# Kernel tuning notes

Measured on AMD Instinct MI355X. Metric: run time of the kernel, lower is better.

Reference implementation:

```python
import jax, jax.numpy as jnp
import numpy as np

CUTOFF = 2.0
LOG2 = float(np.log(2.0))

def ssp(x):
    # shifted softplus: softplus(x) - log(2)
    return jax.nn.softplus(x) - LOG2

def setup_inputs() -> dict:
    key = jax.random.key(0)
    ks = jax.random.split(key, 12)
    N, E, H, F, G = 10000, 320000, 256, 256, 50
    x = jax.random.normal(ks[0], (N, H), dtype=jnp.float32)
    edge_index = jax.random.randint(ks[1], (2, E), 0, N, dtype=jnp.int64)
    edge_weight = jax.random.normal(ks[2], (E, 3), dtype=jnp.float32)
    edge_attr = jax.random.normal(ks[3], (E, G), dtype=jnp.float32)
    s = lambda fan_in: 1.0 / np.sqrt(fan_in)
    mlp_w1 = jax.random.uniform(ks[4], (G, F), jnp.float32, -s(G), s(G))
    mlp_b1 = jax.random.uniform(ks[5], (F,), jnp.float32, -s(G), s(G))
    mlp_w2 = jax.random.uniform(ks[6], (F, F), jnp.float32, -s(F), s(F))
    mlp_b2 = jax.random.uniform(ks[7], (F,), jnp.float32, -s(F), s(F))
    lin1_w = jax.random.uniform(ks[8], (H, F), jnp.float32, -s(H), s(H))
    lin2_w = jax.random.uniform(ks[9], (F, H), jnp.float32, -s(F), s(F))
    lin2_b = jax.random.uniform(ks[10], (H,), jnp.float32, -s(F), s(F))
    return {"x": x, "edge_index": edge_index, "edge_weight": edge_weight,
            "edge_attr": edge_attr, "mlp_w1": mlp_w1, "mlp_b1": mlp_b1,
            "mlp_w2": mlp_w2, "mlp_b2": mlp_b2, "lin1_w": lin1_w,
            "lin2_w": lin2_w, "lin2_b": lin2_b}

def reference(x, edge_index, edge_weight, edge_attr,
              mlp_w1, mlp_b1, mlp_w2, mlp_b2, lin1_w, lin2_w, lin2_b):
    N = x.shape[0]
    # cutoff envelope on edge distances
    distances = jnp.linalg.norm(edge_weight, axis=1)                 # [E]
    C = 0.5 * (jnp.cos(distances * jnp.pi / CUTOFF) + 1.0)
    C = C * (distances <= CUTOFF)                                    # [E]
    # edge filter MLP
    W = ssp(edge_attr @ mlp_w1 + mlp_b1) @ mlp_w2 + mlp_b2           # [E, F]
    W = W * C[:, None]
    i, j = edge_index[0], edge_index[1]
    messages = W * (x[j] @ lin1_w)                                   # [E, F]
    agg = jax.ops.segment_sum(messages, i, num_segments=N)           # [N, F]
    h = ssp(agg @ lin2_w + lin2_b)                                   # [N, H]
    return x + h
```

## Files before the change

kernel.cpp:

```cpp
#include <hip/hip_runtime.h>
#include <hip/hip_bf16.h>
#include <stdint.h>

#define HF 256
#define GG 50

typedef __attribute__((ext_vector_type(8))) short bf16x8;
typedef __attribute__((ext_vector_type(4))) short bf16x4;
typedef __attribute__((ext_vector_type(4))) float f32x4;

__device__ __forceinline__ uint32_t f2bf2u(float a, float b){
    __hip_bfloat162 h = __float22bfloat162_rn(make_float2(a, b));
    union { __hip_bfloat162 h; uint32_t u; } v; v.h = h; return v.u;
}
__device__ __forceinline__ short f2bf(float x){
    union { float f; uint32_t u; } v; v.f = x;
    uint32_t r = (v.u + 0x7FFFu + ((v.u >> 16) & 1u)) >> 16;
    return (short)(uint16_t)r;
}
__device__ __forceinline__ float bf2f(short s){
    union { uint32_t u; float f; } v; v.u = ((uint32_t)(uint16_t)s) << 16;
    return v.f;
}
__device__ __forceinline__ float ssp_f(float x){
    return fmaxf(x, 0.f) + __logf(1.f + __expf(-fabsf(x))) - 0.69314718055994531f;
}

__device__ __forceinline__ void pack_natural(const float* __restrict__ B,
                                             short* __restrict__ Bp,
                                             int idx, int KT, int kmax)
{
    int lane = idx & 63;
    int kt   = (idx >> 6) & (KT - 1);
    int ntg  = idx >> (6 + (KT == 2 ? 1 : 3));
    int col  = ntg * 16 + (lane & 15);
    int k0   = kt * 32 + (lane >> 4) * 8;
    uint32_t u[4];
#pragma unroll
    for (int jj = 0; jj < 4; ++jj) {
        int ka = k0 + 2*jj, kb = k0 + 2*jj + 1;
        float a = (ka < kmax) ? B[(size_t)ka * HF + col] : 0.f;
        float b = (kb < kmax) ? B[(size_t)kb * HF + col] : 0.f;
        u[jj] = f2bf2u(a, b);
    }
    *(uint4*)&Bp[(size_t)idx * 8] = *(uint4*)u;
}

__global__ __launch_bounds__(256)
void prep_kernel(const float* __restrict__ w1, const float* __restrict__ w2,
                 const float* __restrict__ lin1, const float* __restrict__ lin2,
                 short* __restrict__ w1p, short* __restrict__ w2p,
                 short* __restrict__ lin1p, short* __restrict__ lin2p,
                 const float* __restrict__ x, short* __restrict__ x_bf, int nx8,
                 const int* __restrict__ eidx, int* __restrict__ cnt, int E, int gConv)
{
    int b = blockIdx.x, tid = threadIdx.x;
    if (b < 8) {
        pack_natural(w1, w1p, b * 256 + tid, 2, GG);
    } else if (b < 40) {
        int idx = (b - 8) * 256 + tid;
        int lane = idx & 63;
        int kt   = (idx >> 6) & 7;
        int ntg  = idx >> 9;
        int col  = ntg * 16 + (lane & 15);
        int s0   = kt * 32 + (lane >> 4) * 8;
        uint32_t u[4];
#pragma unroll
        for (int jj = 0; jj < 4; ++jj) {
            int sa = s0 + 2*jj, sb = sa + 1;
            int fa = (sa >> 6) * 64 + (sa & 3) * 16 + ((sa & 63) >> 2);
            int fb = (sb >> 6) * 64 + (sb & 3) * 16 + ((sb & 63) >> 2);
            u[jj] = f2bf2u(w2[(size_t)fa * HF + col], w2[(size_t)fb * HF + col]);
        }
        *(uint4*)&w2p[(size_t)idx * 8] = *(uint4*)u;
    } else if (b < 72) {
        pack_natural(lin1, lin1p, (b - 40) * 256 + tid, 8, HF);
    } else if (b < 104) {
        pack_natural(lin2, lin2p, (b - 72) * 256 + tid, 8, HF);
    } else if (b < 104 + gConv) {
        int idx = (b - 104) * 256 + tid;
        if (idx < nx8) {
            const float* xp = x + (size_t)idx * 8;
            float4 p0 = *(const float4*)(xp);
            float4 p1 = *(const float4*)(xp + 4);
            uint32_t u[4] = { f2bf2u(p0.x, p0.y), f2bf2u(p0.z, p0.w),
                              f2bf2u(p1.x, p1.y), f2bf2u(p1.z, p1.w) };
            *(uint4*)&x_bf[(size_t)idx * 8] = *(uint4*)u;
        }
    } else {
        int e = (b - 104 - gConv) * 256 + tid;
        if (e < E) atomicAdd(&cnt[eidx[e]], 1);
    }
}

__global__ __launch_bounds__(256)
void scan_kernel(const int* __restrict__ cnt, int* __restrict__ row,
                 int* __restrict__ cursor, int N, int E)
{
    __shared__ int part[256];
    const int t = threadIdx.x;
    const int CH = (N + 255) / 256;
    int lo = t * CH;
    int hi = min(lo + CH, N);
    int s = 0;
    for (int n = lo; n < hi; ++n) s += cnt[n];
    part[t] = s;
    __syncthreads();
    for (int off = 1; off < 256; off <<= 1) {
        int v = (t >= off) ? part[t - off] : 0;
        __syncthreads();
        part[t] += v;
        __syncthreads();
    }
    int acc = part[t] - s;
    for (int n = lo; n < hi; ++n) {
        row[n] = acc; cursor[n] = acc;
        acc += cnt[n];
    }
    if (t == 255) row[N] = E;
}

__global__ __launch_bounds__(256)
void mid_kernel(const int* __restrict__ eidx, int* __restrict__ cursor,
                int* __restrict__ perm, int E, int gScatter,
                const short* __restrict__ x_bf, const short* __restrict__ lin1p,
                short* __restrict__ y_p, int N)
{
    const int tid = threadIdx.x;
    if ((int)blockIdx.x < gScatter) {
        int e = blockIdx.x * 256 + tid;
        if (e < E) {
            int pos = atomicAdd(&cursor[eidx[e]], 1);
            perm[pos] = e;
        }
        return;
    }
    const int blk  = blockIdx.x - gScatter;
    const int lane = tid & 63;
    const int w    = tid >> 6;
    const int l15  = lane & 15;
    const int quad = lane >> 4;
    const int row0 = blk * 64;

    f32x4 acc[4][4];
#pragma unroll
    for (int mt = 0; mt < 4; ++mt)
#pragma unroll
        for (int nt = 0; nt < 4; ++nt)
            acc[mt][nt] = (f32x4){0.f, 0.f, 0.f, 0.f};

#pragma unroll 2
    for (int kt = 0; kt < 8; ++kt) {
        bf16x8 af[4];
#pragma unroll
        for (int mt = 0; mt < 4; ++mt) {
            int r = row0 + mt * 16 + l15;
            int rl = (r < N) ? r : 0;
            af[mt] = *(const bf16x8*)&x_bf[(size_t)rl * HF + kt * 32 + quad * 8];
        }
#pragma unroll
        for (int nt = 0; nt < 4; ++nt) {
            bf16x8 bfr = *(const bf16x8*)&lin1p[(size_t)(((w * 4 + nt) * 8 + kt) * 64 + lane) * 8];
#pragma unroll
            for (int mt = 0; mt < 4; ++mt)
                acc[mt][nt] = __builtin_amdgcn_mfma_f32_16x16x32_bf16(af[mt], bfr, acc[mt][nt], 0, 0, 0);
        }
    }
#pragma unroll
    for (int mt = 0; mt < 4; ++mt) {
#pragma unroll
        for (int r = 0; r < 4; ++r) {
            int row = row0 + mt * 16 + quad * 4 + r;
            if (row < N) {
                uint2 u = make_uint2(f2bf2u(acc[mt][0][r], acc[mt][1][r]),
                                     f2bf2u(acc[mt][2][r], acc[mt][3][r]));
                *(uint2*)&y_p[(size_t)row * HF + w * 64 + l15 * 4] = u;
            }
        }
    }
}

__global__ __launch_bounds__(256)
void node2_kernel(const float* __restrict__ agg, const short* __restrict__ lin2p,
                  const float* __restrict__ bias, const float* __restrict__ x,
                  float* __restrict__ out, int N)
{
    const int tid  = threadIdx.x;
    const int lane = tid & 63;
    const int w    = tid >> 6;
    const int l15  = lane & 15;
    const int quad = lane >> 4;
    const int row0 = blockIdx.x * 64;

    f32x4 acc[4][4];
#pragma unroll
    for (int mt = 0; mt < 4; ++mt)
#pragma unroll
        for (int nt = 0; nt < 4; ++nt)
            acc[mt][nt] = (f32x4){0.f, 0.f, 0.f, 0.f};

#pragma unroll 2
    for (int kt = 0; kt < 8; ++kt) {
        bf16x8 af[4];
#pragma unroll
        for (int mt = 0; mt < 4; ++mt) {
            int r = row0 + mt * 16 + l15;
            int rl = (r < N) ? r : 0;
            const float* ap = agg + (size_t)rl * HF + kt * 32 + quad * 8;
            float4 p0 = *(const float4*)(ap);
            float4 p1 = *(const float4*)(ap + 4);
            union { uint32_t u[4]; bf16x8 v; } c;
            c.u[0] = f2bf2u(p0.x, p0.y); c.u[1] = f2bf2u(p0.z, p0.w);
            c.u[2] = f2bf2u(p1.x, p1.y); c.u[3] = f2bf2u(p1.z, p1.w);
            af[mt] = c.v;
        }
#pragma unroll
        for (int nt = 0; nt < 4; ++nt) {
            bf16x8 bfr = *(const bf16x8*)&lin2p[(size_t)(((w * 4 + nt) * 8 + kt) * 64 + lane) * 8];
#pragma unroll
            for (int mt = 0; mt < 4; ++mt)
                acc[mt][nt] = __builtin_amdgcn_mfma_f32_16x16x32_bf16(af[mt], bfr, acc[mt][nt], 0, 0, 0);
        }
    }
    float bs[4];
#pragma unroll
    for (int nt = 0; nt < 4; ++nt) bs[nt] = bias[w * 64 + nt * 16 + l15];
#pragma unroll
    for (int mt = 0; mt < 4; ++mt) {
#pragma unroll
        for (int r = 0; r < 4; ++r) {
            int row = row0 + mt * 16 + quad * 4 + r;
            if (row < N) {
#pragma unroll
                for (int nt = 0; nt < 4; ++nt) {
                    int f = w * 64 + nt * 16 + l15;
                    float v = ssp_f(acc[mt][nt][r] + bs[nt]) + x[(size_t)row * HF + f];
                    out[(size_t)row * HF + f] = v;
                }
            }
        }
    }
}

__global__ __launch_bounds__(256, 3)
void edge_mfma(const float* __restrict__ ea, const int* __restrict__ eidx,
               const float* __restrict__ ew,
               const short* __restrict__ w1p, const float* __restrict__ b1,
               const short* __restrict__ w2p, const float* __restrict__ b2,
               const short* __restrict__ y_p, const int* __restrict__ perm,
               const int* __restrict__ rowp,
               float* __restrict__ agg, int E)
{
    __shared__ short smem[21504];
    short* ea_b = smem;
    short* hid  = smem + 4608;
    short* msgT = smem;
    __shared__ int s_e[64], s_i[64], s_j[64];
    __shared__ float s_c[64];
    __shared__ unsigned long long s_bmask;

    const int tid  = threadIdx.x;
    const int lane = tid & 63;
    const int w    = tid >> 6;
    const int l15  = lane & 15;
    const int quad = lane >> 4;
    const int e0   = blockIdx.x * 64;

    if (tid < 64) {
        int p = e0 + tid;
        int e = 0, iv = -1, jv = 0;
        float c = 0.f;
        if (p < E) {
            e  = perm[p];
            iv = eidx[e];
            jv = eidx[E + e];
            float d0 = ew[e*3+0], d1 = ew[e*3+1], d2 = ew[e*3+2];
            float d = sqrtf(d0*d0 + d1*d1 + d2*d2);
            c = (d <= 2.0f) ? 0.5f * (__cosf(d * 1.57079632679489662f) + 1.0f) : 0.f;
        }
        s_e[tid] = e; s_i[tid] = iv; s_j[tid] = jv; s_c[tid] = c;
        int ivn = __shfl_down(iv, 1);
        bool flag = (tid == 63) || (iv != ivn);
        unsigned long long m = __ballot(flag);
        if (tid == 0) s_bmask = m;
    }
    __syncthreads();

    for (int idx = tid; idx < 64 * 25; idx += 256) {
        int e = idx / 25, p = idx - e * 25;
        const float* sp = ea + (size_t)s_e[e] * GG + p * 2;
        float2 v = *(const float2*)sp;
        *(uint32_t*)&ea_b[e * 72 + p * 2] = f2bf2u(v.x, v.y);
    }
    for (int idx = tid; idx < 64 * 7; idx += 256) {
        int e = idx / 7, q = idx - e * 7;
        *(uint32_t*)&ea_b[e * 72 + 50 + q * 2] = 0u;
    }
    __syncthreads();

    f32x4 acc1[4][4];
#pragma unroll
    for (int mt = 0; mt < 4; ++mt)
#pragma unroll
        for (int nt = 0; nt < 4; ++nt)
            acc1[mt][nt] = (f32x4){0.f, 0.f, 0.f, 0.f};

#pragma unroll
    for (int kt = 0; kt < 2; ++kt) {
        bf16x8 af[4];
#pragma unroll
        for (int mt = 0; mt < 4; ++mt)
            af[mt] = *(bf16x8*)&ea_b[(mt * 16 + l15) * 72 + kt * 32 + quad * 8];
#pragma unroll
        for (int nt = 0; nt < 4; ++nt) {
            bf16x8 bfr = *(const bf16x8*)&w1p[(size_t)(((w * 4 + nt) * 2 + kt) * 64 + lane) * 8];
#pragma unroll
            for (int mt = 0; mt < 4; ++mt)
                acc1[mt][nt] = __builtin_amdgcn_mfma_f32_16x16x32_bf16(af[mt], bfr, acc1[mt][nt], 0, 0, 0);
        }
    }

    float bias1[4];
#pragma unroll
    for (int nt = 0; nt < 4; ++nt) bias1[nt] = b1[w * 64 + nt * 16 + l15];
#pragma unroll
    for (int mt = 0; mt < 4; ++mt) {
#pragma unroll
        for (int r = 0; r < 4; ++r) {
            int e = mt * 16 + quad * 4 + r;
            float v0 = ssp_f(acc1[mt][0][r] + bias1[0]);
            float v1 = ssp_f(acc1[mt][1][r] + bias1[1]);
            float v2 = ssp_f(acc1[mt][2][r] + bias1[2]);
            float v3 = ssp_f(acc1[mt][3][r] + bias1[3]);
            uint2 u = make_uint2(f2bf2u(v0, v1), f2bf2u(v2, v3));
            *(uint2*)&hid[e * 264 + w * 64 + l15 * 4] = u;
        }
    }
    __syncthreads();

    bf16x4 yv[4][4];
#pragma unroll
    for (int mt = 0; mt < 4; ++mt)
#pragma unroll
        for (int r = 0; r < 4; ++r) {
            int e = mt * 16 + quad * 4 + r;
            yv[mt][r] = *(const bf16x4*)&y_p[(size_t)s_j[e] * HF + w * 64 + l15 * 4];
        }

    f32x4 acc2[4][4];
#pragma unroll
    for (int mt = 0; mt < 4; ++mt)
#pragma unroll
        for (int nt = 0; nt < 4; ++nt)
            acc2[mt][nt] = (f32x4){0.f, 0.f, 0.f, 0.f};

#pragma unroll 2
    for (int kt = 0; kt < 8; ++kt) {
        bf16x8 af[4];
#pragma unroll
        for (int mt = 0; mt < 4; ++mt)
            af[mt] = *(bf16x8*)&hid[(mt * 16 + l15) * 264 + kt * 32 + quad * 8];
#pragma unroll
        for (int nt = 0; nt < 4; ++nt) {
            bf16x8 bfr = *(const bf16x8*)&w2p[(size_t)(((w * 4 + nt) * 8 + kt) * 64 + lane) * 8];
#pragma unroll
            for (int mt = 0; mt < 4; ++mt)
                acc2[mt][nt] = __builtin_amdgcn_mfma_f32_16x16x32_bf16(af[mt], bfr, acc2[mt][nt], 0, 0, 0);
        }
    }
    __syncthreads();

    float bias2[4];
#pragma unroll
    for (int nt = 0; nt < 4; ++nt) bias2[nt] = b2[w * 64 + nt * 16 + l15];
    float cs[4][4];
#pragma unroll
    for (int mt = 0; mt < 4; ++mt)
#pragma unroll
        for (int r = 0; r < 4; ++r)
            cs[mt][r] = s_c[mt * 16 + quad * 4 + r];
#pragma unroll
    for (int mt = 0; mt < 4; ++mt) {
#pragma unroll
        for (int nt = 0; nt < 4; ++nt) {
            int col = w * 64 + nt * 16 + l15;
            float v0 = (acc2[mt][nt][0] + bias2[nt]) * cs[mt][0] * bf2f(yv[mt][0][nt]);
            float v1 = (acc2[mt][nt][1] + bias2[nt]) * cs[mt][1] * bf2f(yv[mt][1][nt]);
            float v2 = (acc2[mt][nt][2] + bias2[nt]) * cs[mt][2] * bf2f(yv[mt][2][nt]);
            float v3 = (acc2[mt][nt][3] + bias2[nt]) * cs[mt][3] * bf2f(yv[mt][3][nt]);
            uint2 u = make_uint2(f2bf2u(v0, v1), f2bf2u(v2, v3));
            *(uint2*)&msgT[col * 68 + mt * 16 + quad * 4] = u;
        }
    }
    __syncthreads();

    {
        unsigned long long bm = s_bmask;
        unsigned mlo = __builtin_amdgcn_readfirstlane((unsigned)bm);
        unsigned mhi = __builtin_amdgcn_readfirstlane((unsigned)(bm >> 32));
        const int col = tid;
        float sum = 0.f;
#pragma unroll
        for (int ch = 0; ch < 8; ++ch) {
            bf16x8 v = *(bf16x8*)&msgT[col * 68 + ch * 8];
#pragma unroll
            for (int j = 0; j < 8; ++j) {
                int e = ch * 8 + j;
                sum += bf2f(v[j]);
                unsigned bit = (e < 32) ? ((mlo >> e) & 1u) : ((mhi >> (e - 32)) & 1u);
                if (bit) {
                    int node = __builtin_amdgcn_readfirstlane(s_i[e]);
                    if (node >= 0) {
                        int lo = rowp[node], hi = rowp[node + 1];
                        float* ap = agg + (size_t)node * HF + col;
                        if (lo >= e0 && hi <= e0 + 64) *ap = sum;
                        else atomicAdd(ap, sum);
                    }
                    sum = 0.f;
                }
            }
        }
    }
}

extern "C" void kernel_launch(void* const* d_in, const int* in_sizes, int n_in,
                              void* d_out, int out_size, void* d_ws, size_t ws_size,
                              hipStream_t stream)
{
    const float* x     = (const float*)d_in[0];
    const int*   eidx  = (const int*)  d_in[1];
    const float* ew    = (const float*)d_in[2];
    const float* ea    = (const float*)d_in[3];
    const float* w1    = (const float*)d_in[4];
    const float* b1    = (const float*)d_in[5];
    const float* w2    = (const float*)d_in[6];
    const float* b2    = (const float*)d_in[7];
    const float* lin1  = (const float*)d_in[8];
    const float* lin2  = (const float*)d_in[9];
    const float* lin2b = (const float*)d_in[10];
    float* out = (float*)d_out;

    const int N = in_sizes[0] / HF;
    const int E = in_sizes[2] / 3;

    const size_t fN = (size_t)N * HF;
    float* agg    = (float*)d_ws;
    short* y_p    = (short*)(agg + fN);
    short* x_bf   = y_p + fN;
    int*   cnt    = (int*)(x_bf + fN);
    int*   row    = cnt + N;
    int*   cursor = row + (N + 8);
    int*   perm   = cursor + N;
    short* w1p    = (short*)(((uintptr_t)(perm + E) + 255) & ~(uintptr_t)255);
    short* w2p    = w1p + 16384;
    short* lin1p  = w2p + 65536;
    short* lin2p  = lin1p + 65536;

    hipMemsetAsync(cnt, 0, (size_t)N * sizeof(int), stream);
    hipMemsetAsync(agg, 0, fN * sizeof(float), stream);

    const int nx8   = (int)(fN / 8);
    const int gConv = (nx8 + 255) / 256;
    const int gHist = (E + 255) / 256;
    prep_kernel<<<dim3(104 + gConv + gHist), dim3(256), 0, stream>>>(
        w1, w2, lin1, lin2, w1p, w2p, lin1p, lin2p, x, x_bf, nx8, eidx, cnt, E, gConv);

    scan_kernel<<<dim3(1), dim3(256), 0, stream>>>(cnt, row, cursor, N, E);

    const int gScatter = (E + 255) / 256;
    const int gNode    = (N + 63) / 64;
    mid_kernel<<<dim3(gScatter + gNode), dim3(256), 0, stream>>>(
        eidx, cursor, perm, E, gScatter, x_bf, lin1p, y_p, N);

    edge_mfma<<<dim3((E + 63) / 64), dim3(256), 0, stream>>>(
        ea, eidx, ew, w1p, b1, w2p, b2, y_p, perm, row, agg, E);

    node2_kernel<<<dim3(gNode), dim3(256), 0, stream>>>(
        agg, lin2p, lin2b, x, out, N);
}
```

Measured before the change: 346.6 us.

## Do segment reduction with MFMA selection matrix and fold agg zeroing into prep

Replaces the per-column serial scan over 64 edges, which did scalar atomics or stores at each run boundary, with an MFMA product of the transposed message tile and a 0/1 run-selection matrix built in shared memory. Each run's sum then comes out of the matrix unit and is written as float4 stores, or atomics when the run crosses the block. Run node ids and a completeness flag are precomputed per block. The separate memset of agg is folded into the prep kernel as extra zeroing blocks, removing one launch. This adds an extra loop iteration with barriers whenever a block holds more than 16 runs, and random node ids likely give many runs per 64 edges, so the new path may do more work than the old scan.

```diff
diff --git a/kernel.cpp b/kernel.cpp
--- a/kernel.cpp
+++ b/kernel.cpp
@@ -12,11 +12,6 @@
 __device__ __forceinline__ uint32_t f2bf2u(float a, float b){
     __hip_bfloat162 h = __float22bfloat162_rn(make_float2(a, b));
     union { __hip_bfloat162 h; uint32_t u; } v; v.h = h; return v.u;
-}
-__device__ __forceinline__ short f2bf(float x){
-    union { float f; uint32_t u; } v; v.f = x;
-    uint32_t r = (v.u + 0x7FFFu + ((v.u >> 16) & 1u)) >> 16;
-    return (short)(uint16_t)r;
 }
 __device__ __forceinline__ float bf2f(short s){
     union { uint32_t u; float f; } v; v.u = ((uint32_t)(uint16_t)s) << 16;
@@ -38,7 +33,7 @@
     uint32_t u[4];
 #pragma unroll
     for (int jj = 0; jj < 4; ++jj) {
-        int ka = k0 + 2*jj, kb = k0 + 2*jj + 1;
+        int ka = k0 + 2*jj, kb = ka + 1;
         float a = (ka < kmax) ? B[(size_t)ka * HF + col] : 0.f;
         float b = (kb < kmax) ? B[(size_t)kb * HF + col] : 0.f;
         u[jj] = f2bf2u(a, b);
@@ -52,7 +47,8 @@
                  short* __restrict__ w1p, short* __restrict__ w2p,
                  short* __restrict__ lin1p, short* __restrict__ lin2p,
                  const float* __restrict__ x, short* __restrict__ x_bf, int nx8,
-                 const int* __restrict__ eidx, int* __restrict__ cnt, int E, int gConv)
+                 const int* __restrict__ eidx, int* __restrict__ cnt, int E,
+                 float* __restrict__ agg, int nAgg4, int gConv, int gHist)
 {
     int b = blockIdx.x, tid = threadIdx.x;
     if (b < 8) {
@@ -87,9 +83,12 @@
                               f2bf2u(p1.x, p1.y), f2bf2u(p1.z, p1.w) };
             *(uint4*)&x_bf[(size_t)idx * 8] = *(uint4*)u;
         }
-    } else {
+    } else if (b < 104 + gConv + gHist) {
         int e = (b - 104 - gConv) * 256 + tid;
         if (e < E) atomicAdd(&cnt[eidx[e]], 1);
+    } else {
+        int idx = (b - 104 - gConv - gHist) * 256 + tid;
+        if (idx < nAgg4) ((float4*)agg)[idx] = make_float4(0.f, 0.f, 0.f, 0.f);
     }
 }
 
@@ -146,8 +145,7 @@
 #pragma unroll
     for (int mt = 0; mt < 4; ++mt)
 #pragma unroll
-        for (int nt = 0; nt < 4; ++nt)
-            acc[mt][nt] = (f32x4){0.f, 0.f, 0.f, 0.f};
+        for (int nt = 0; nt < 4; ++nt) acc[mt][nt] = (f32x4){0.f,0.f,0.f,0.f};
 
 #pragma unroll 2
     for (int kt = 0; kt < 8; ++kt) {
@@ -160,7 +158,7 @@
         }
 #pragma unroll
         for (int nt = 0; nt < 4; ++nt) {
-            bf16x8 bfr = *(const bf16x8*)&lin1p[(size_t)(((w * 4 + nt) * 8 + kt) * 64 + lane) * 8];
+            bf16x8 bfr = *(const bf16x8*)&lin1p[(size_t)(((w*4+nt)*8+kt)*64+lane)*8];
 #pragma unroll
             for (int mt = 0; mt < 4; ++mt)
                 acc[mt][nt] = __builtin_amdgcn_mfma_f32_16x16x32_bf16(af[mt], bfr, acc[mt][nt], 0, 0, 0);
@@ -196,8 +194,7 @@
 #pragma unroll
     for (int mt = 0; mt < 4; ++mt)
 #pragma unroll
-        for (int nt = 0; nt < 4; ++nt)
-            acc[mt][nt] = (f32x4){0.f, 0.f, 0.f, 0.f};
+        for (int nt = 0; nt < 4; ++nt) acc[mt][nt] = (f32x4){0.f,0.f,0.f,0.f};
 
 #pragma unroll 2
     for (int kt = 0; kt < 8; ++kt) {
@@ -216,7 +213,7 @@
         }
 #pragma unroll
         for (int nt = 0; nt < 4; ++nt) {
-            bf16x8 bfr = *(const bf16x8*)&lin2p[(size_t)(((w * 4 + nt) * 8 + kt) * 64 + lane) * 8];
+            bf16x8 bfr = *(const bf16x8*)&lin2p[(size_t)(((w*4+nt)*8+kt)*64+lane)*8];
 #pragma unroll
             for (int mt = 0; mt < 4; ++mt)
                 acc[mt][nt] = __builtin_amdgcn_mfma_f32_16x16x32_bf16(af[mt], bfr, acc[mt][nt], 0, 0, 0);
@@ -255,9 +252,13 @@
     short* ea_b = smem;
     short* hid  = smem + 4608;
     short* msgT = smem;
+    short* St   = smem + 18432;
     __shared__ int s_e[64], s_i[64], s_j[64];
     __shared__ float s_c[64];
+    __shared__ int s_runnode[64];
+    __shared__ unsigned char s_runcomp[64];
     __shared__ unsigned long long s_bmask;
+    __shared__ int s_runcnt;
 
     const int tid  = threadIdx.x;
     const int lane = tid & 63;
@@ -267,11 +268,11 @@
     const int e0   = blockIdx.x * 64;
 
     if (tid < 64) {
-        int p = e0 + tid;
+        int pp = e0 + tid;
         int e = 0, iv = -1, jv = 0;
         float c = 0.f;
-        if (p < E) {
-            e  = perm[p];
+        if (pp < E) {
+            e  = perm[pp];
             iv = eidx[e];
             jv = eidx[E + e];
             float d0 = ew[e*3+0], d1 = ew[e*3+1], d2 = ew[e*3+2];
@@ -282,15 +283,25 @@
         int ivn = __shfl_down(iv, 1);
         bool flag = (tid == 63) || (iv != ivn);
         unsigned long long m = __ballot(flag);
-        if (tid == 0) s_bmask = m;
+        if (flag) {
+            int rid = (int)__popcll(m & ((1ull << tid) - 1ull));
+            s_runnode[rid] = iv;
+            int comp = 0;
+            if (iv >= 0) {
+                int lo = rowp[iv], hi = rowp[iv + 1];
+                comp = (lo >= e0 && hi <= e0 + 64) ? 1 : 0;
+            }
+            s_runcomp[rid] = (unsigned char)comp;
+        }
+        if (tid == 0) { s_bmask = m; s_runcnt = (int)__popcll(m); }
     }
     __syncthreads();
 
     for (int idx = tid; idx < 64 * 25; idx += 256) {
-        int e = idx / 25, p = idx - e * 25;
-        const float* sp = ea + (size_t)s_e[e] * GG + p * 2;
+        int e = idx / 25, q = idx - e * 25;
+        const float* sp = ea + (size_t)s_e[e] * GG + q * 2;
         float2 v = *(const float2*)sp;
-        *(uint32_t*)&ea_b[e * 72 + p * 2] = f2bf2u(v.x, v.y);
+        *(uint32_t*)&ea_b[e * 72 + q * 2] = f2bf2u(v.x, v.y);
     }
     for (int idx = tid; idx < 64 * 7; idx += 256) {
         int e = idx / 7, q = idx - e * 7;
@@ -302,8 +313,7 @@
 #pragma unroll
     for (int mt = 0; mt < 4; ++mt)
 #pragma unroll
-        for (int nt = 0; nt < 4; ++nt)
-            acc1[mt][nt] = (f32x4){0.f, 0.f, 0.f, 0.f};
+        for (int nt = 0; nt < 4; ++nt) acc1[mt][nt] = (f32x4){0.f,0.f,0.f,0.f};
 
 #pragma unroll
     for (int kt = 0; kt < 2; ++kt) {
@@ -313,7 +323,7 @@
             af[mt] = *(bf16x8*)&ea_b[(mt * 16 + l15) * 72 + kt * 32 + quad * 8];
 #pragma unroll
         for (int nt = 0; nt < 4; ++nt) {
-            bf16x8 bfr = *(const bf16x8*)&w1p[(size_t)(((w * 4 + nt) * 2 + kt) * 64 + lane) * 8];
+            bf16x8 bfr = *(const bf16x8*)&w1p[(size_t)(((w*4+nt)*2+kt)*64+lane)*8];
 #pragma unroll
             for (int mt = 0; mt < 4; ++mt)
                 acc1[mt][nt] = __builtin_amdgcn_mfma_f32_16x16x32_bf16(af[mt], bfr, acc1[mt][nt], 0, 0, 0);
@@ -351,8 +361,7 @@
 #pragma unroll
     for (int mt = 0; mt < 4; ++mt)
 #pragma unroll
-        for (int nt = 0; nt < 4; ++nt)
-            acc2[mt][nt] = (f32x4){0.f, 0.f, 0.f, 0.f};
+        for (int nt = 0; nt < 4; ++nt) acc2[mt][nt] = (f32x4){0.f,0.f,0.f,0.f};
 
 #pragma unroll 2
     for (int kt = 0; kt < 8; ++kt) {
@@ -362,7 +371,7 @@
             af[mt] = *(bf16x8*)&hid[(mt * 16 + l15) * 264 + kt * 32 + quad * 8];
 #pragma unroll
         for (int nt = 0; nt < 4; ++nt) {
-            bf16x8 bfr = *(const bf16x8*)&w2p[(size_t)(((w * 4 + nt) * 8 + kt) * 64 + lane) * 8];
+            bf16x8 bfr = *(const bf16x8*)&w2p[(size_t)(((w*4+nt)*8+kt)*64+lane)*8];
 #pragma unroll
             for (int mt = 0; mt < 4; ++mt)
                 acc2[mt][nt] = __builtin_amdgcn_mfma_f32_16x16x32_bf16(af[mt], bfr, acc2[mt][nt], 0, 0, 0);
@@ -389,34 +398,66 @@
             float v2 = (acc2[mt][nt][2] + bias2[nt]) * cs[mt][2] * bf2f(yv[mt][2][nt]);
             float v3 = (acc2[mt][nt][3] + bias2[nt]) * cs[mt][3] * bf2f(yv[mt][3][nt]);
             uint2 u = make_uint2(f2bf2u(v0, v1), f2bf2u(v2, v3));
-            *(uint2*)&msgT[col * 68 + mt * 16 + quad * 4] = u;
-        }
-    }
-    __syncthreads();
-
+            *(uint2*)&msgT[col * 72 + mt * 16 + quad * 4] = u;
+        }
+    }
     {
         unsigned long long bm = s_bmask;
-        unsigned mlo = __builtin_amdgcn_readfirstlane((unsigned)bm);
-        unsigned mhi = __builtin_amdgcn_readfirstlane((unsigned)(bm >> 32));
-        const int col = tid;
-        float sum = 0.f;
-#pragma unroll
-        for (int ch = 0; ch < 8; ++ch) {
-            bf16x8 v = *(bf16x8*)&msgT[col * 68 + ch * 8];
-#pragma unroll
-            for (int j = 0; j < 8; ++j) {
-                int e = ch * 8 + j;
-                sum += bf2f(v[j]);
-                unsigned bit = (e < 32) ? ((mlo >> e) & 1u) : ((mhi >> (e - 32)) & 1u);
-                if (bit) {
-                    int node = __builtin_amdgcn_readfirstlane(s_i[e]);
-                    if (node >= 0) {
-                        int lo = rowp[node], hi = rowp[node + 1];
-                        float* ap = agg + (size_t)node * HF + col;
-                        if (lo >= e0 && hi <= e0 + 64) *ap = sum;
-                        else atomicAdd(ap, sum);
+        int e   = tid & 63;
+        int rb  = tid >> 6;
+        int rid = (int)__popcll(bm & ((1ull << e) - 1ull));
+#pragma unroll
+        for (int q = 0; q < 4; ++q) {
+            int r = rb + q * 4;
+            St[r * 64 + e] = (rid == r) ? (short)0x3F80 : (short)0;
+        }
+    }
+    __syncthreads();
+
+    const int runcnt = s_runcnt;
+    for (int ntg = 0; ntg * 16 < runcnt; ++ntg) {
+        if (ntg > 0) {
+            __syncthreads();
+            unsigned long long bm = s_bmask;
+            int e   = tid & 63;
+            int rb  = tid >> 6;
+            int rid = (int)__popcll(bm & ((1ull << e) - 1ull));
+#pragma unroll
+            for (int q = 0; q < 4; ++q) {
+                int r = rb + q * 4;
+                St[r * 64 + e] = (rid == ntg * 16 + r) ? (short)0x3F80 : (short)0;
+            }
+            __syncthreads();
+        }
+        f32x4 acc3[4];
+#pragma unroll
+        for (int mt = 0; mt < 4; ++mt) acc3[mt] = (f32x4){0.f,0.f,0.f,0.f};
+#pragma unroll
+        for (int kt = 0; kt < 2; ++kt) {
+            bf16x8 bS = *(bf16x8*)&St[l15 * 64 + kt * 32 + quad * 8];
+#pragma unroll
+            for (int mt = 0; mt < 4; ++mt) {
+                bf16x8 af = *(bf16x8*)&msgT[(w*64 + mt*16 + l15) * 72 + kt*32 + quad*8];
+                acc3[mt] = __builtin_amdgcn_mfma_f32_16x16x32_bf16(af, bS, acc3[mt], 0, 0, 0);
+            }
+        }
+        int r = ntg * 16 + l15;
+        if (r < runcnt) {
+            int node = s_runnode[r];
+            if (node >= 0) {
+                float* ap = agg + (size_t)node * HF + w * 64 + quad * 4;
+                if (s_runcomp[r]) {
+#pragma unroll
+                    for (int mt = 0; mt < 4; ++mt) {
+                        float4 v = make_float4(acc3[mt][0], acc3[mt][1], acc3[mt][2], acc3[mt][3]);
+                        *(float4*)(ap + mt * 16) = v;
                     }
-                    sum = 0.f;
+                } else {
+#pragma unroll
+                    for (int mt = 0; mt < 4; ++mt)
+#pragma unroll
+                        for (int g = 0; g < 4; ++g)
+                            atomicAdd(ap + mt * 16 + g, acc3[mt][g]);
                 }
             }
         }
@@ -457,13 +498,15 @@
     short* lin2p  = lin1p + 65536;
 
     hipMemsetAsync(cnt, 0, (size_t)N * sizeof(int), stream);
-    hipMemsetAsync(agg, 0, fN * sizeof(float), stream);
 
     const int nx8   = (int)(fN / 8);
+    const int nAgg4 = (int)(fN / 4);
     const int gConv = (nx8 + 255) / 256;
     const int gHist = (E + 255) / 256;
-    prep_kernel<<<dim3(104 + gConv + gHist), dim3(256), 0, stream>>>(
-        w1, w2, lin1, lin2, w1p, w2p, lin1p, lin2p, x, x_bf, nx8, eidx, cnt, E, gConv);
+    const int gZero = (nAgg4 + 255) / 256;
+    prep_kernel<<<dim3(104 + gConv + gHist + gZero), dim3(256), 0, stream>>>(
+        w1, w2, lin1, lin2, w1p, w2p, lin1p, lin2p, x, x_bf, nx8,
+        eidx, cnt, E, agg, nAgg4, gConv, gHist);
 
     scan_kernel<<<dim3(1), dim3(256), 0, stream>>>(cnt, row, cursor, N, E);
 
```

Result: no change. 345.9 us (-0.2%).
